# Optimization experiments

Hardware: AMD Instinct MI355X
Metric: run time of the kernel (lower is better)

## Reference

```python
import jax, jax.numpy as jnp
import numpy as np

B, C, Hh, Ww = 4, 128, 256, 256
NH = 4          # num_heads
DK = C // NH    # 32
PH = PW = 8     # patchsize[log2(4)] = (8,8) for every head


def setup_inputs() -> dict:
    key = jax.random.key(0)
    ks = jax.random.split(key, 12)
    s = 0.02
    return {
        "x": jax.random.normal(ks[0], (B, C, Hh, Ww), jnp.float32),
        "m": jax.random.uniform(ks[1], (B, 1, Hh, Ww), jnp.float32),
        "wq": jax.random.normal(ks[2], (C, C), jnp.float32) * s,
        "bq": jnp.zeros((C,), jnp.float32),
        "wk": jax.random.normal(ks[3], (C, C), jnp.float32) * s,
        "bk": jnp.zeros((C,), jnp.float32),
        "wv": jax.random.normal(ks[4], (C, C), jnp.float32) * s,
        "bv": jnp.zeros((C,), jnp.float32),
        "wo": jax.random.normal(ks[5], (C, C, 3, 3), jnp.float32) * s,
        "bo": jnp.zeros((C,), jnp.float32),
    }


def _conv1x1(x, w, b):
    # x: [b,c,h,w], w: [o,c]
    return jnp.einsum('bchw,oc->bohw', x, w) + b[None, :, None, None]


def _to_windows(t, b, oh, ow):
    # [b,NH,DK,h,w] -> [b,NH,oh*ow, DK*PH*PW]  (matches torch permute(0,2,4,1,3,5))
    t = t.reshape(b, NH, DK, oh, PH, ow, PW)
    t = t.transpose(0, 1, 3, 5, 2, 4, 6)
    return t.reshape(b, NH, oh * ow, DK * PH * PW)


def reference(x, m, wq, bq, wk, bk, wv, bv, wo, bo):
    b, c, h, w = x.shape
    oh, ow = h // PH, w // PW
    q = _conv1x1(x, wq, bq).reshape(b, NH, DK, h, w)
    k = _conv1x1(x, wk, bk).reshape(b, NH, DK, h, w)
    v = _conv1x1(x, wv, bv).reshape(b, NH, DK, h, w)
    qw = _to_windows(q, b, oh, ow)  # [b,NH,nw,d]
    kw = _to_windows(k, b, oh, ow)
    vw = _to_windows(v, b, oh, ow)
    d = qw.shape[-1]
    # NOTE: original torch calls scores.masked_fill(m, -1e9) without assignment,
    # so the mask is a no-op; we faithfully omit it from the math.
    scores = jnp.einsum('bhnd,bhmd->bhnm', qw, kw) / jnp.sqrt(jnp.float32(d))
    p = jax.nn.softmax(scores, axis=-1)
    y = jnp.einsum('bhnm,bhmd->bhnd', p, vw)
    # inverse window partition -> [b, C, h, w] (head chunks concat along channel)
    y = y.reshape(b, NH, oh, ow, DK, PH, PW)
    y = y.transpose(0, 1, 4, 2, 5, 3, 6).reshape(b, c, h, w)
    # output: 3x3 conv with reflect padding, then LeakyReLU(0.2)
    yp = jnp.pad(y, ((0, 0), (0, 0), (1, 1), (1, 1)), mode='reflect')
    out = jax.lax.conv_general_dilated(
        yp, wo, window_strides=(1, 1), padding='VALID',
        dimension_numbers=('NCHW', 'OIHW', 'NCHW'))
    out = out + bo[None, :, None, None]
    return jnp.where(out > 0, out, 0.2 * out)
```

## Files before the change

### kernel.cpp

```cpp
#include <hip/hip_runtime.h>

typedef float f32x4 __attribute__((ext_vector_type(4)));
typedef __bf16 bf16x8 __attribute__((ext_vector_type(8)));

#define IMH 256
#define IMW 256
#define NCH 128
#define NHEAD 4
#define NWIN 1024
#define DWIN 2048
#define HW (IMH*IMW)

__device__ __forceinline__ unsigned short bf16u(float f) {
  __bf16 h = (__bf16)f;
  return __builtin_bit_cast(unsigned short, h);
}
__device__ __forceinline__ f32x4 fzero() { f32x4 z = {0.f, 0.f, 0.f, 0.f}; return z; }

__global__ void k_prep_w(const float* __restrict__ wq, const float* __restrict__ wk,
                         const float* __restrict__ wv, __bf16* __restrict__ wt) {
  int i = blockIdx.x * 256 + threadIdx.x;
  if (i < 16384) {
    wt[i]         = (__bf16)wq[i];
    wt[i + 16384] = (__bf16)wk[i];
    wt[i + 32768] = (__bf16)wv[i];
  }
}

__global__ void k_prep_wo(const float* __restrict__ wo, __bf16* __restrict__ wot) {
  int i = blockIdx.x * 256 + threadIdx.x;
  if (i < 9*16384) {
    int kk = i >> 14;
    int oc = i & 16383;
    wot[i] = (__bf16)wo[oc*9 + kk];
  }
}

__global__ __launch_bounds__(512)
void k_qkv(const float* __restrict__ x, const __bf16* __restrict__ wt,
           const float* __restrict__ bq, const float* __restrict__ bk,
           const float* __restrict__ bv,
           __bf16* __restrict__ qw, __bf16* __restrict__ kw, __bf16* __restrict__ vt) {
  __shared__ __align__(16) unsigned short xt[256*128];
  const int bidx = blockIdx.x;
  const int b = bidx >> 8, h = bidx & 255;
  const int py = h & 7, oy = h >> 3;
  const int t = threadIdx.x;
  {
    const int w = t & 255, half = t >> 8;
    const float* xb = x + (size_t)(b*NCH)*HW + (size_t)h*IMW + w;
    #pragma unroll 8
    for (int i = 0; i < 32; ++i) {
      int c = half*64 + 2*i;
      float v0 = xb[(size_t)c*HW];
      float v1 = xb[(size_t)(c+1)*HW];
      unsigned int pk = (unsigned int)bf16u(v0) | ((unsigned int)bf16u(v1) << 16);
      *(unsigned int*)((char*)xt + (w*256 + ((c*2) ^ ((w&7)<<4)))) = pk;
    }
  }
  __syncthreads();
  const int lane = t & 63, wid = t >> 6;
  const int wm = wid >> 2, wn = wid & 3;
  const int l15 = lane & 15, l4 = lane >> 4;
  for (int mat = 0; mat < 3; ++mat) {
    const __bf16* wmat = wt + mat*16384;
    const float* bias = (mat == 0) ? bq : ((mat == 1) ? bk : bv);
    f32x4 acc[4][4];
    #pragma unroll
    for (int i = 0; i < 4; ++i)
      #pragma unroll
      for (int j = 0; j < 4; ++j) acc[i][j] = fzero();
    #pragma unroll
    for (int kc = 0; kc < 4; ++kc) {
      bf16x8 a[4], bb[4];
      #pragma unroll
      for (int i = 0; i < 4; ++i) {
        int o = wm*64 + i*16 + l15;
        a[i] = *(const bf16x8*)(wmat + o*128 + kc*32 + l4*8);
      }
      #pragma unroll
      for (int j = 0; j < 4; ++j) {
        int wc = wn*64 + j*16 + l15;
        bb[j] = *(const bf16x8*)((const char*)xt + (wc*256 + ((kc*64 + l4*16) ^ ((wc&7)<<4))));
      }
      #pragma unroll
      for (int i = 0; i < 4; ++i)
        #pragma unroll
        for (int j = 0; j < 4; ++j)
          acc[i][j] = __builtin_amdgcn_mfma_f32_16x16x32_bf16(a[i], bb[j], acc[i][j], 0, 0, 0);
    }
    if (mat < 2) {
      __bf16* dst = (mat == 0) ? qw : kw;
      #pragma unroll
      for (int i = 0; i < 4; ++i)
        #pragma unroll
        for (int r = 0; r < 4; ++r) {
          int o = wm*64 + i*16 + l4*4 + r;
          float bi = bias[o];
          int nh = o >> 5, dk = o & 31;
          #pragma unroll
          for (int j = 0; j < 4; ++j) {
            int wcol = wn*64 + j*16 + l15;
            int ox = wcol >> 3, px = wcol & 7;
            size_t idx = (size_t)((b*NHEAD + nh)*NWIN + oy*32 + ox)*DWIN + dk*64 + py*8 + px;
            dst[idx] = (__bf16)(acc[i][j][r] + bi);
          }
        }
    } else {
      __syncthreads();
      unsigned short* rp = xt;
      #pragma unroll
      for (int i = 0; i < 4; ++i)
        #pragma unroll
        for (int r = 0; r < 4; ++r) {
          int o = wm*64 + i*16 + l4*4 + r;
          float bi = bias[o];
          #pragma unroll
          for (int j = 0; j < 4; ++j) {
            int wcol = wn*64 + j*16 + l15;
            rp[o*256 + wcol] = bf16u(acc[i][j][r] + bi);
          }
        }
      __syncthreads();
      #pragma unroll
      for (int it = 0; it < 2; ++it) {
        int u = t + it*512;
        int o = u >> 3, px = u & 7;
        int nh = o >> 5, dk = o & 31;
        unsigned short tmp[32];
        #pragma unroll
        for (int ox = 0; ox < 32; ++ox) tmp[ox] = rp[o*256 + ox*8 + px];
        __bf16* dstp = vt + (size_t)((b*NHEAD + nh)*DWIN + dk*64 + py*8 + px)*NWIN + oy*32;
        #pragma unroll
        for (int qq = 0; qq < 4; ++qq) {
          uint4 val;
          val.x = (unsigned int)tmp[qq*8+0] | ((unsigned int)tmp[qq*8+1] << 16);
          val.y = (unsigned int)tmp[qq*8+2] | ((unsigned int)tmp[qq*8+3] << 16);
          val.z = (unsigned int)tmp[qq*8+4] | ((unsigned int)tmp[qq*8+5] << 16);
          val.w = (unsigned int)tmp[qq*8+6] | ((unsigned int)tmp[qq*8+7] << 16);
          ((uint4*)dstp)[qq] = val;
        }
      }
    }
  }
}

__device__ __forceinline__ void gemm_tile(const __bf16* __restrict__ A,
                                          const __bf16* __restrict__ B,
                                          const int lda, const int ldb, const int NT,
                                          unsigned short* Asm, unsigned short* Bsm,
                                          f32x4 (&acc)[4][4]) {
  const int t = threadIdx.x;
  const int lane = t & 63, wid = t >> 6;
  const int wm = wid >> 1, wn = wid & 1;
  const int l15 = lane & 15, l4 = lane >> 4;
  const int u0 = t, u1 = t + 256;
  const int ra0 = u0 >> 2, ca0 = u0 & 3;
  const int ra1 = u1 >> 2, ca1 = u1 & 3;
  uint4 ar0 = *(const uint4*)(A + ra0*lda + ca0*8);
  uint4 ar1 = *(const uint4*)(A + ra1*lda + ca1*8);
  uint4 br0 = *(const uint4*)(B + ra0*ldb + ca0*8);
  uint4 br1 = *(const uint4*)(B + ra1*ldb + ca1*8);
  for (int kt = 0; kt < NT; ++kt) {
    __syncthreads();
    *(uint4*)(Asm + u0*8) = ar0;
    *(uint4*)(Asm + u1*8) = ar1;
    *(uint4*)(Bsm + u0*8) = br0;
    *(uint4*)(Bsm + u1*8) = br1;
    __syncthreads();
    if (kt + 1 < NT) {
      int k0 = (kt+1)*32;
      ar0 = *(const uint4*)(A + ra0*lda + k0 + ca0*8);
      ar1 = *(const uint4*)(A + ra1*lda + k0 + ca1*8);
      br0 = *(const uint4*)(B + ra0*ldb + k0 + ca0*8);
      br1 = *(const uint4*)(B + ra1*ldb + k0 + ca1*8);
    }
    bf16x8 a[4], bb[4];
    #pragma unroll
    for (int i = 0; i < 4; ++i)
      a[i] = *(const bf16x8*)((const char*)Asm + (wm*64 + i*16 + l15)*64 + l4*16);
    #pragma unroll
    for (int j = 0; j < 4; ++j)
      bb[j] = *(const bf16x8*)((const char*)Bsm + (wn*64 + j*16 + l15)*64 + l4*16);
    #pragma unroll
    for (int i = 0; i < 4; ++i)
      #pragma unroll
      for (int j = 0; j < 4; ++j)
        acc[i][j] = __builtin_amdgcn_mfma_f32_16x16x32_bf16(a[i], bb[j], acc[i][j], 0, 0, 0);
  }
}

__global__ __launch_bounds__(256)
void k_scores(const __bf16* __restrict__ qw, const __bf16* __restrict__ kw,
              float* __restrict__ S) {
  __shared__ __align__(16) unsigned short Asm[4096], Bsm[4096];
  const int bnh = blockIdx.y;
  const int mt = blockIdx.x >> 3, nt = blockIdx.x & 7;
  const __bf16* A = qw + (size_t)bnh*NWIN*DWIN + (size_t)mt*128*DWIN;
  const __bf16* B = kw + (size_t)bnh*NWIN*DWIN + (size_t)nt*128*DWIN;
  f32x4 acc[4][4];
  #pragma unroll
  for (int i = 0; i < 4; ++i)
    #pragma unroll
    for (int j = 0; j < 4; ++j) acc[i][j] = fzero();
  gemm_tile(A, B, DWIN, DWIN, 64, Asm, Bsm, acc);
  const float scale = 0.022097086912079608f;
  const int t = threadIdx.x, lane = t & 63, wid = t >> 6;
  const int wm = wid >> 1, wn = wid & 1, l15 = lane & 15, l4 = lane >> 4;
  float* Sb = S + (size_t)bnh*NWIN*NWIN + (size_t)(mt*128)*NWIN + nt*128;
  #pragma unroll
  for (int i = 0; i < 4; ++i)
    #pragma unroll
    for (int r = 0; r < 4; ++r) {
      int row = wm*64 + i*16 + l4*4 + r;
      #pragma unroll
      for (int j = 0; j < 4; ++j) {
        int col = wn*64 + j*16 + l15;
        Sb[(size_t)row*NWIN + col] = acc[i][j][r] * scale;
      }
    }
}

__global__ __launch_bounds__(256)
void k_softmax(const float* __restrict__ S, __bf16* __restrict__ P) {
  __shared__ float red[8];
  const int row = blockIdx.x;
  const int t = threadIdx.x;
  const float4 v = ((const float4*)(S + (size_t)row*NWIN))[t];
  float m = fmaxf(fmaxf(v.x, v.y), fmaxf(v.z, v.w));
  for (int off = 1; off < 64; off <<= 1) m = fmaxf(m, __shfl_xor(m, off));
  const int wid = t >> 6, lane = t & 63;
  if (lane == 0) red[wid] = m;
  __syncthreads();
  m = fmaxf(fmaxf(red[0], red[1]), fmaxf(red[2], red[3]));
  float e0 = __expf(v.x - m), e1 = __expf(v.y - m), e2 = __expf(v.z - m), e3 = __expf(v.w - m);
  float s = e0 + e1 + e2 + e3;
  for (int off = 1; off < 64; off <<= 1) s += __shfl_xor(s, off);
  if (lane == 0) red[4 + wid] = s;
  __syncthreads();
  s = red[4] + red[5] + red[6] + red[7];
  float inv = 1.0f / s;
  ushort4 o;
  o.x = bf16u(e0*inv); o.y = bf16u(e1*inv); o.z = bf16u(e2*inv); o.w = bf16u(e3*inv);
  ((ushort4*)((unsigned short*)P + (size_t)row*NWIN))[t] = o;
}

__global__ __launch_bounds__(256)
void k_pv(const __bf16* __restrict__ P, const __bf16* __restrict__ vt,
          __bf16* __restrict__ y) {
  __shared__ __align__(16) unsigned short Asm[4096], Bsm[4096];
  const int bnh = blockIdx.y;
  const int b = bnh >> 2, nh = bnh & 3;
  const int mt = blockIdx.x >> 4, nt = blockIdx.x & 15;
  const __bf16* A = P  + (size_t)bnh*NWIN*NWIN + (size_t)mt*128*NWIN;
  const __bf16* B = vt + (size_t)bnh*DWIN*NWIN + (size_t)nt*128*NWIN;
  f32x4 acc[4][4];
  #pragma unroll
  for (int i = 0; i < 4; ++i)
    #pragma unroll
    for (int j = 0; j < 4; ++j) acc[i][j] = fzero();
  gemm_tile(A, B, NWIN, NWIN, 32, Asm, Bsm, acc);
  const int t = threadIdx.x, lane = t & 63, wid = t >> 6;
  const int wm = wid >> 1, wn = wid & 1, l15 = lane & 15, l4 = lane >> 4;
  #pragma unroll
  for (int i = 0; i < 4; ++i)
    #pragma unroll
    for (int r = 0; r < 4; ++r) {
      int n = mt*128 + wm*64 + i*16 + l4*4 + r;
      int oyy = n >> 5, oxx = n & 31;
      #pragma unroll
      for (int j = 0; j < 4; ++j) {
        int d = nt*128 + wn*64 + j*16 + l15;
        int dk = d >> 6, pyy = (d >> 3) & 7, pxx = d & 7;
        int c = nh*32 + dk, hh = oyy*8 + pyy, ww = oxx*8 + pxx;
        y[(size_t)((b*NCH + c)*IMH + hh)*IMW + ww] = (__bf16)acc[i][j][r];
      }
    }
}

__global__ __launch_bounds__(256)
void k_conv(const __bf16* __restrict__ y, const __bf16* __restrict__ wot,
            const float* __restrict__ bo, float* __restrict__ out) {
  __shared__ __align__(16) unsigned short ylds[3*132*64];
  const int bid = blockIdx.x;
  const int half = bid & 1, h = (bid >> 1) & 255, b = bid >> 9;
  const int w0 = half * 128;
  const int t = threadIdx.x;
  const int hm1 = (h == 0) ? 1 : h - 1;
  const int hp1 = (h == 255) ? 254 : h + 1;
  const int lane = t & 63, wid = t >> 6;
  const int wm = wid >> 1, wn = wid & 1, l15 = lane & 15, l4 = lane >> 4;
  f32x4 acc[4][4];
  #pragma unroll
  for (int i = 0; i < 4; ++i)
    #pragma unroll
    for (int j = 0; j < 4; ++j) acc[i][j] = fzero();
  const unsigned short* yu = (const unsigned short*)y;
  for (int cc = 0; cc < 4; ++cc) {
    __syncthreads();
    for (int u = t; u < 3*32*130; u += 256) {
      int wl = u % 130;
      int rc = u / 130;
      int c = rc & 31, rowr = rc >> 5;
      int hh = (rowr == 0) ? hm1 : ((rowr == 1) ? h : hp1);
      int gw = w0 - 1 + wl;
      gw = (gw < 0) ? 1 : ((gw > 255) ? 254 : gw);
      unsigned short val = yu[(size_t)((b*NCH + cc*32 + c)*IMH + hh)*IMW + gw];
      int R = rowr*132 + wl;
      *(unsigned short*)((char*)ylds + R*128 + ((c*2) ^ ((R&7)<<4))) = val;
    }
    __syncthreads();
    #pragma unroll
    for (int kk = 0; kk < 9; ++kk) {
      const int ky = kk / 3, kx = kk % 3;
      bf16x8 a[4], bb[4];
      #pragma unroll
      for (int i = 0; i < 4; ++i) {
        int o = wm*64 + i*16 + l15;
        a[i] = *(const bf16x8*)(wot + ((size_t)kk*128 + o)*128 + cc*32 + l4*8);
      }
      #pragma unroll
      for (int j = 0; j < 4; ++j) {
        int px = wn*64 + j*16 + l15;
        int R = ky*132 + px + kx;
        bb[j] = *(const bf16x8*)((const char*)ylds + R*128 + ((l4*16) ^ ((R&7)<<4)));
      }
      #pragma unroll
      for (int i = 0; i < 4; ++i)
        #pragma unroll
        for (int j = 0; j < 4; ++j)
          acc[i][j] = __builtin_amdgcn_mfma_f32_16x16x32_bf16(a[i], bb[j], acc[i][j], 0, 0, 0);
    }
  }
  #pragma unroll
  for (int i = 0; i < 4; ++i)
    #pragma unroll
    for (int r = 0; r < 4; ++r) {
      int o = wm*64 + i*16 + l4*4 + r;
      float bi = bo[o];
      #pragma unroll
      for (int j = 0; j < 4; ++j) {
        int px = wn*64 + j*16 + l15;
        float v = acc[i][j][r] + bi;
        v = (v > 0.f) ? v : 0.2f * v;
        out[(size_t)((b*NCH + o)*IMH + h)*IMW + w0 + px] = v;
      }
    }
}

extern "C" void kernel_launch(void* const* d_in, const int* in_sizes, int n_in,
                              void* d_out, int out_size, void* d_ws, size_t ws_size,
                              hipStream_t stream) {
  (void)in_sizes; (void)n_in; (void)out_size; (void)ws_size;
  const float* x  = (const float*)d_in[0];
  const float* wq = (const float*)d_in[2];
  const float* bq = (const float*)d_in[3];
  const float* wk = (const float*)d_in[4];
  const float* bk = (const float*)d_in[5];
  const float* wv = (const float*)d_in[6];
  const float* bv = (const float*)d_in[7];
  const float* wo = (const float*)d_in[8];
  const float* bo = (const float*)d_in[9];
  float* out = (float*)d_out;
  char* ws = (char*)d_ws;
  __bf16* qw  = (__bf16*)(ws + 0);
  __bf16* kw  = (__bf16*)(ws + 67108864);
  __bf16* vt  = (__bf16*)(ws + 134217728);
  float*  S   = (float*)(ws + 201326592);
  __bf16* P   = (__bf16*)(ws + 0);
  __bf16* yb  = (__bf16*)(ws + 201326592);
  __bf16* wt  = (__bf16*)(ws + 201326592);
  __bf16* wot = (__bf16*)(ws + 67108864);

  k_prep_w<<<64, 256, 0, stream>>>(wq, wk, wv, wt);
  k_qkv<<<1024, 512, 0, stream>>>(x, wt, bq, bk, bv, qw, kw, vt);
  k_scores<<<dim3(64, 16), 256, 0, stream>>>(qw, kw, S);
  k_prep_wo<<<576, 256, 0, stream>>>(wo, wot);
  k_softmax<<<16384, 256, 0, stream>>>(S, P);
  k_pv<<<dim3(128, 16), 256, 0, stream>>>(P, vt, yb);
  k_conv<<<2048, 256, 0, stream>>>(yb, wot, bo, out);
}
```

Measured before the change: 568.2 us.

## Use channel-last y layout, permuted V feature order, and padded LDS GEMM tiles

Reorders the V-transpose feature dimension so that the PV output for each head can be written in a pixel-major, 32-channel-contiguous layout. The conv kernel then loads its input with 16-byte vector reads instead of scalar gathers. The shared GEMM tile and the conv LDS tile move from XOR swizzles to an 80-byte padded row stride to avoid bank conflicts. The qkv epilogue staging buffer gains an XOR swizzle. The cost is slightly more LDS per block and a layout coupling across three kernels.

```diff
diff --git a/kernel.cpp b/kernel.cpp
--- a/kernel.cpp
+++ b/kernel.cpp
@@ -118,7 +118,8 @@
           #pragma unroll
           for (int j = 0; j < 4; ++j) {
             int wcol = wn*64 + j*16 + l15;
-            rp[o*256 + wcol] = bf16u(acc[i][j][r] + bi);
+            *(unsigned short*)((char*)rp + o*512 + ((wcol*2) ^ ((o&7)<<4))) =
+                bf16u(acc[i][j][r] + bi);
           }
         }
       __syncthreads();
@@ -129,8 +130,9 @@
         int nh = o >> 5, dk = o & 31;
         unsigned short tmp[32];
         #pragma unroll
-        for (int ox = 0; ox < 32; ++ox) tmp[ox] = rp[o*256 + ox*8 + px];
-        __bf16* dstp = vt + (size_t)((b*NHEAD + nh)*DWIN + dk*64 + py*8 + px)*NWIN + oy*32;
+        for (int ox = 0; ox < 32; ++ox)
+          tmp[ox] = *(const unsigned short*)((const char*)rp + o*512 + (((ox*8+px)*2) ^ ((o&7)<<4)));
+        __bf16* dstp = vt + ((size_t)(b*NHEAD + nh)*DWIN + (py*8+px)*32 + dk)*NWIN + oy*32;
         #pragma unroll
         for (int qq = 0; qq < 4; ++qq) {
           uint4 val;
@@ -163,10 +165,10 @@
   uint4 br1 = *(const uint4*)(B + ra1*ldb + ca1*8);
   for (int kt = 0; kt < NT; ++kt) {
     __syncthreads();
-    *(uint4*)(Asm + u0*8) = ar0;
-    *(uint4*)(Asm + u1*8) = ar1;
-    *(uint4*)(Bsm + u0*8) = br0;
-    *(uint4*)(Bsm + u1*8) = br1;
+    *(uint4*)((char*)Asm + ra0*80 + ca0*16) = ar0;
+    *(uint4*)((char*)Asm + ra1*80 + ca1*16) = ar1;
+    *(uint4*)((char*)Bsm + ra0*80 + ca0*16) = br0;
+    *(uint4*)((char*)Bsm + ra1*80 + ca1*16) = br1;
     __syncthreads();
     if (kt + 1 < NT) {
       int k0 = (kt+1)*32;
@@ -178,10 +180,10 @@
     bf16x8 a[4], bb[4];
     #pragma unroll
     for (int i = 0; i < 4; ++i)
-      a[i] = *(const bf16x8*)((const char*)Asm + (wm*64 + i*16 + l15)*64 + l4*16);
+      a[i] = *(const bf16x8*)((const char*)Asm + (wm*64 + i*16 + l15)*80 + l4*16);
     #pragma unroll
     for (int j = 0; j < 4; ++j)
-      bb[j] = *(const bf16x8*)((const char*)Bsm + (wn*64 + j*16 + l15)*64 + l4*16);
+      bb[j] = *(const bf16x8*)((const char*)Bsm + (wn*64 + j*16 + l15)*80 + l4*16);
     #pragma unroll
     for (int i = 0; i < 4; ++i)
       #pragma unroll
@@ -193,7 +195,7 @@
 __global__ __launch_bounds__(256)
 void k_scores(const __bf16* __restrict__ qw, const __bf16* __restrict__ kw,
               float* __restrict__ S) {
-  __shared__ __align__(16) unsigned short Asm[4096], Bsm[4096];
+  __shared__ __align__(16) unsigned short Asm[5120], Bsm[5120];
   const int bnh = blockIdx.y;
   const int mt = blockIdx.x >> 3, nt = blockIdx.x & 7;
   const __bf16* A = qw + (size_t)bnh*NWIN*DWIN + (size_t)mt*128*DWIN;
@@ -247,8 +249,8 @@
 
 __global__ __launch_bounds__(256)
 void k_pv(const __bf16* __restrict__ P, const __bf16* __restrict__ vt,
-          __bf16* __restrict__ y) {
-  __shared__ __align__(16) unsigned short Asm[4096], Bsm[4096];
+          __bf16* __restrict__ y3) {
+  __shared__ __align__(16) unsigned short Asm[5120], Bsm[5120];
   const int bnh = blockIdx.y;
   const int b = bnh >> 2, nh = bnh & 3;
   const int mt = blockIdx.x >> 4, nt = blockIdx.x & 15;
@@ -262,6 +264,8 @@
   gemm_tile(A, B, NWIN, NWIN, 32, Asm, Bsm, acc);
   const int t = threadIdx.x, lane = t & 63, wid = t >> 6;
   const int wm = wid >> 1, wn = wid & 1, l15 = lane & 15, l4 = lane >> 4;
+  unsigned short* yu = (unsigned short*)y3;
+  const size_t cbase = (size_t)(b*NHEAD + nh)*65536*32;
   #pragma unroll
   for (int i = 0; i < 4; ++i)
     #pragma unroll
@@ -270,18 +274,18 @@
       int oyy = n >> 5, oxx = n & 31;
       #pragma unroll
       for (int j = 0; j < 4; ++j) {
-        int d = nt*128 + wn*64 + j*16 + l15;
-        int dk = d >> 6, pyy = (d >> 3) & 7, pxx = d & 7;
-        int c = nh*32 + dk, hh = oyy*8 + pyy, ww = oxx*8 + pxx;
-        y[(size_t)((b*NCH + c)*IMH + hh)*IMW + ww] = (__bf16)acc[i][j][r];
+        int pp = nt*4 + wn*2 + (j >> 1);
+        int dk = (j & 1)*16 + l15;
+        int hh = oyy*8 + (pp >> 3), ww = oxx*8 + (pp & 7);
+        yu[cbase + ((size_t)hh*256 + ww)*32 + dk] = bf16u(acc[i][j][r]);
       }
     }
 }
 
 __global__ __launch_bounds__(256)
-void k_conv(const __bf16* __restrict__ y, const __bf16* __restrict__ wot,
+void k_conv(const __bf16* __restrict__ y3, const __bf16* __restrict__ wot,
             const float* __restrict__ bo, float* __restrict__ out) {
-  __shared__ __align__(16) unsigned short ylds[3*132*64];
+  __shared__ __align__(16) unsigned short ylds[15840];
   const int bid = blockIdx.x;
   const int half = bid & 1, h = (bid >> 1) & 255, b = bid >> 9;
   const int w0 = half * 128;
@@ -295,19 +299,27 @@
   for (int i = 0; i < 4; ++i)
     #pragma unroll
     for (int j = 0; j < 4; ++j) acc[i][j] = fzero();
-  const unsigned short* yu = (const unsigned short*)y;
+  const unsigned short* yu = (const unsigned short*)y3;
   for (int cc = 0; cc < 4; ++cc) {
+    const size_t cbase = (size_t)(b*NHEAD + cc)*65536*32;
     __syncthreads();
-    for (int u = t; u < 3*32*130; u += 256) {
-      int wl = u % 130;
-      int rc = u / 130;
-      int c = rc & 31, rowr = rc >> 5;
+    #pragma unroll
+    for (int it = 0; it < 6; ++it) {
+      int u = it*256 + t;
+      int seg = u & 3, wl = (u >> 2) & 127, rowr = u >> 9;
       int hh = (rowr == 0) ? hm1 : ((rowr == 1) ? h : hp1);
       int gw = w0 - 1 + wl;
       gw = (gw < 0) ? 1 : ((gw > 255) ? 254 : gw);
-      unsigned short val = yu[(size_t)((b*NCH + cc*32 + c)*IMH + hh)*IMW + gw];
-      int R = rowr*132 + wl;
-      *(unsigned short*)((char*)ylds + R*128 + ((c*2) ^ ((R&7)<<4))) = val;
+      uint4 val = *(const uint4*)(yu + cbase + ((size_t)hh*256 + gw)*32 + seg*8);
+      *(uint4*)((char*)ylds + (rowr*132 + wl)*80 + seg*16) = val;
+    }
+    if (t < 24) {
+      int seg = t & 3, wl = 128 + ((t >> 2) & 1), rowr = t >> 3;
+      int hh = (rowr == 0) ? hm1 : ((rowr == 1) ? h : hp1);
+      int gw = w0 - 1 + wl;
+      gw = (gw < 0) ? 1 : ((gw > 255) ? 254 : gw);
+      uint4 val = *(const uint4*)(yu + cbase + ((size_t)hh*256 + gw)*32 + seg*8);
+      *(uint4*)((char*)ylds + (rowr*132 + wl)*80 + seg*16) = val;
     }
     __syncthreads();
     #pragma unroll
@@ -323,7 +335,7 @@
       for (int j = 0; j < 4; ++j) {
         int px = wn*64 + j*16 + l15;
         int R = ky*132 + px + kx;
-        bb[j] = *(const bf16x8*)((const char*)ylds + R*128 + ((l4*16) ^ ((R&7)<<4)));
+        bb[j] = *(const bf16x8*)((const char*)ylds + R*80 + l4*16);
       }
       #pragma unroll
       for (int i = 0; i < 4; ++i)
@@ -368,7 +380,7 @@
   __bf16* vt  = (__bf16*)(ws + 134217728);
   float*  S   = (float*)(ws + 201326592);
   __bf16* P   = (__bf16*)(ws + 0);
-  __bf16* yb  = (__bf16*)(ws + 201326592);
+  __bf16* y3  = (__bf16*)(ws + 201326592);
   __bf16* wt  = (__bf16*)(ws + 201326592);
   __bf16* wot = (__bf16*)(ws + 67108864);
 
@@ -377,6 +389,6 @@
   k_scores<<<dim3(64, 16), 256, 0, stream>>>(qw, kw, S);
   k_prep_wo<<<576, 256, 0, stream>>>(wo, wot);
   k_softmax<<<16384, 256, 0, stream>>>(S, P);
-  k_pv<<<dim3(128, 16), 256, 0, stream>>>(P, vt, yb);
-  k_conv<<<2048, 256, 0, stream>>>(yb, wot, bo, out);
-}
+  k_pv<<<dim3(128, 16), 256, 0, stream>>>(P, vt, y3);
+  k_conv<<<2048, 256, 0, stream>>>(y3, wot, bo, out);
+}
```

Result: slower. 636.2 us (+12.0%).
